# Optimization experiments

Hardware: AMD Instinct MI355X
Metric: run time of the kernel (lower is better)

## Reference

```python
import jax, jax.numpy as jnp
import numpy as np

B, PLEN, D = 32, 1024, 256


def setup_inputs() -> dict:
    key = jax.random.key(0)
    ks = jax.random.split(key, 8)
    u = lambda k, shape: jax.random.uniform(k, shape, jnp.float32, -0.05, 0.05)
    return {
        "P": jax.random.normal(ks[0], (B, PLEN, D), jnp.float32),
        "w_itr_att": u(ks[1], (3 * D,)),
        "w1": u(ks[2], (2 * D, D)),
        "w2": u(ks[3], (2 * D, D)),
        "w3": u(ks[4], (2 * D, D)),
        "b1": u(ks[5], (D,)),
        "b2": u(ks[6], (D,)),
        "b3": u(ks[7], (D,)),
    }


def reference(P, w_itr_att, w1, w2, w3, b1, b2, b3):
    d = P.shape[-1]
    # alpha(a,b) = w_itr_att . [a ; b ; a*b]; split w into the three d-chunks
    wa, wb, wc = w_itr_att[:d], w_itr_att[d:2 * d], w_itr_att[2 * d:]
    # pairwise score A[b,i,j] = wa.P_i + wb.P_j + wc.(P_i * P_j)
    sa = P @ wa                                   # (b, p)
    sb = P @ wb                                   # (b, p)
    A = sa[:, :, None] + sb[:, None, :] + jnp.einsum('bid,bjd->bij', P * wc, P)
    itr_attn = jnp.einsum('bij,bjd->bid', jax.nn.softmax(A, axis=2), P)
    cat = jnp.concatenate([P, itr_attn], axis=-1)  # (b, p, 2d)
    z = jnp.tanh(cat @ w1 + b1)
    r = jax.nn.sigmoid(cat @ w2 + b2)
    f = jax.nn.sigmoid(cat @ w3 + b3)
    return r * P + f * z
```

## Files before the change

kernel.cpp:

```cpp
#include <hip/hip_runtime.h>
#include <hip/hip_bf16.h>

typedef unsigned short u16;
typedef unsigned int   u32;

using bf16x8 = __attribute__((ext_vector_type(8))) short;
using f32x4  = __attribute__((ext_vector_type(4))) float;

#define NB 32
#define NP 1024
#define ND 256

__device__ __forceinline__ u16 f2bf(float x){
  u32 u = __float_as_uint(x);
  u += 0x7FFFu + ((u >> 16) & 1u);
  return (u16)(u >> 16);
}

__device__ __forceinline__ float bf2f(u16 x){
  return __uint_as_float((u32)x << 16);
}

__device__ __forceinline__ void glds16(const void* g, void* l){
  __builtin_amdgcn_global_load_lds((const __attribute__((address_space(1))) void*)g,
                                   (__attribute__((address_space(3))) void*)l, 16, 0, 0);
}

__global__ void prep_rows(const float* __restrict__ P, const float* __restrict__ wi,
                          u16* __restrict__ Pbf, float* __restrict__ sbv){
  const int row  = blockIdx.x * 4 + (threadIdx.x >> 6);
  const int lane = threadIdx.x & 63;
  const float4 p  = *(const float4*)(P  + (size_t)row * ND + lane * 4);
  const float4 wb = *(const float4*)(wi + ND + lane * 4);
  ushort4 pb;
  pb.x = f2bf(p.x); pb.y = f2bf(p.y); pb.z = f2bf(p.z); pb.w = f2bf(p.w);
  *(ushort4*)(Pbf + (size_t)row * ND + lane * 4) = pb;
  float s = p.x*wb.x + p.y*wb.y + p.z*wb.z + p.w*wb.w;
  #pragma unroll
  for (int m = 1; m < 64; m <<= 1) s += __shfl_xor(s, m, 64);
  if (lane == 0) sbv[row] = s;
}

__global__ void prep_w(const float* __restrict__ w1, const float* __restrict__ w2,
                       const float* __restrict__ w3, u16* __restrict__ Wp){
  const int t = blockIdx.x;
  const float* w = (t < 16) ? w1 : ((t < 32) ? w2 : w3);
  const int tid = threadIdx.x;
  #pragma unroll
  for (int j = 0; j < 4; ++j){
    int item = tid + 256 * j;
    int c = item >> 6, lane = item & 63;
    int ncol = ((t & 15) << 4) + (lane & 15);
    int k0 = 32 * c + 8 * (lane >> 4);
    u16 tmp[8];
    #pragma unroll
    for (int e = 0; e < 8; ++e) tmp[e] = f2bf(w[(size_t)(k0 + e) * 256 + ncol]);
    *(uint4*)(Wp + ((size_t)(t * 16 + c) * 64 + lane) * 8) = *(uint4*)tmp;
  }
}

__global__ void transpose_p(const u16* __restrict__ Pbf, u16* __restrict__ PbfT){
  const int b = blockIdx.z, jt = blockIdx.x, dt = blockIdx.y;
  __shared__ u16 T[64][72];
  const int tid = threadIdx.x;
  #pragma unroll
  for (int it = 0; it < 2; ++it){
    int cc = tid + 256 * it;
    int j = cc >> 3, c8 = cc & 7;
    uint4 v = *(const uint4*)(Pbf + ((size_t)b * NP + jt * 64 + j) * ND + dt * 64 + c8 * 8);
    *(uint4*)&T[j][c8 * 8] = v;
  }
  __syncthreads();
  #pragma unroll
  for (int it = 0; it < 2; ++it){
    int cc = tid + 256 * it;
    int d = cc >> 3, c8 = cc & 7;
    u16 tmp[8];
    #pragma unroll
    for (int k = 0; k < 8; ++k) tmp[k] = T[c8 * 8 + k][d];
    *(uint4*)(PbfT + ((size_t)b * ND + dt * 64 + d) * NP + jt * 64 + c8 * 8) = *(uint4*)tmp;
  }
}

__launch_bounds__(128, 2)
__global__ void attn_kernel(const float* __restrict__ P, const float* __restrict__ wi,
                            const u16* __restrict__ Pbf, const u16* __restrict__ PbfT,
                            const float* __restrict__ sbv, u16* __restrict__ attnb){
  const int p    = blockIdx.x;
  const int bid  = ((p & 7) << 7) | (p >> 3);
  const int b    = bid >> 5;
  const int q0   = (bid & 31) << 5;
  const int tid  = threadIdx.x;
  const int wave = tid >> 6, lane = tid & 63, lo = lane & 15, hi = lane >> 4;

  __shared__ __align__(16) u16 KtA[32 * 256];
  __shared__ __align__(16) u16 VtA[256 * 32];
  __shared__ __align__(16) u16 Sp[2][16][40];
  char* KtB = (char*)KtA;
  char* VtB = (char*)VtA;

  bf16x8 qf[8];
  {
    const int qrow = q0 + wave * 16 + lo;
    const float* prow = P  + ((size_t)b * NP + qrow) * ND;
    const float* wcp  = wi + 512;
    #pragma unroll
    for (int c = 0; c < 8; ++c){
      const int d0 = 32 * c + 8 * hi;
      float4 a  = *(const float4*)(prow + d0);
      float4 a2 = *(const float4*)(prow + d0 + 4);
      float4 wa  = *(const float4*)(wcp + d0);
      float4 wa2 = *(const float4*)(wcp + d0 + 4);
      bf16x8 q;
      q[0]=(short)f2bf(a.x*wa.x);  q[1]=(short)f2bf(a.y*wa.y);
      q[2]=(short)f2bf(a.z*wa.z);  q[3]=(short)f2bf(a.w*wa.w);
      q[4]=(short)f2bf(a2.x*wa2.x); q[5]=(short)f2bf(a2.y*wa2.y);
      q[6]=(short)f2bf(a2.z*wa2.z); q[7]=(short)f2bf(a2.w*wa2.w);
      qf[c] = q;
    }
  }

  f32x4 of[16];
  #pragma unroll
  for (int t = 0; t < 16; ++t) of[t] = (f32x4){0.f,0.f,0.f,0.f};
  float mx[4] = {-1e30f,-1e30f,-1e30f,-1e30f};
  float ls[4] = {0.f,0.f,0.f,0.f};

  const u16* kslab = Pbf  + (size_t)b * NP * ND;
  const u16* vslab = PbfT + (size_t)b * ND * NP;

  auto stageK = [&](int kt){
    const int kbase = kt * 32;
    #pragma unroll
    for (int it = 0; it < 8; ++it){
      int off = it * 2048 + tid * 16;
      int j   = off >> 9;
      int ck  = ((off >> 4) & 31) ^ (j & 7);
      glds16((const char*)(kslab + (size_t)(kbase + j) * ND + ck * 8), KtB + off);
    }
  };
  auto stageV = [&](int kt){
    const int kbase = kt * 32;
    #pragma unroll
    for (int it = 0; it < 8; ++it){
      int off = it * 2048 + tid * 16;
      int d   = off >> 6;
      int kc  = ((off >> 4) & 3) ^ (d & 3);
      glds16((const char*)(vslab + (size_t)d * NP + kbase + kc * 8), VtB + off);
    }
  };

  float sbc[2], sbn[2];
  stageK(0);
  stageV(0);
  #pragma unroll
  for (int nt = 0; nt < 2; ++nt) sbc[nt] = sbv[(size_t)b * NP + nt * 16 + lo];
  __syncthreads();

  for (int kt = 0; kt < 32; ++kt){
    f32x4 s[2];
    __builtin_amdgcn_s_setprio(1);
    #pragma unroll
    for (int nt = 0; nt < 2; ++nt){
      f32x4 acc = (f32x4){0.f,0.f,0.f,0.f};
      #pragma unroll
      for (int c = 0; c < 8; ++c){
        int j  = nt * 16 + lo;
        int ad = j * 512 + (((4 * c + hi) ^ (j & 7)) << 4);
        bf16x8 kf = *(const bf16x8*)(KtB + ad);
        acc = __builtin_amdgcn_mfma_f32_16x16x32_bf16(qf[c], kf, acc, 0, 0, 0);
      }
      s[nt] = acc;
    }
    __builtin_amdgcn_s_setprio(0);
    #pragma unroll
    for (int nt = 0; nt < 2; ++nt){
      float sv = sbc[nt];
      #pragma unroll
      for (int r = 0; r < 4; ++r) s[nt][r] += sv;
    }

    __syncthreads();
    if (kt < 31) stageK(kt + 1);

    float md = -1e30f;
    #pragma unroll
    for (int nt = 0; nt < 2; ++nt)
      #pragma unroll
      for (int r = 0; r < 4; ++r) md = fmaxf(md, s[nt][r] - mx[r]);
    if (!__all(md <= 8.f)){
      float scale[4];
      #pragma unroll
      for (int r = 0; r < 4; ++r){
        float v = fmaxf(s[0][r], s[1][r]);
        v = fmaxf(v, __shfl_xor(v, 1, 64));
        v = fmaxf(v, __shfl_xor(v, 2, 64));
        v = fmaxf(v, __shfl_xor(v, 4, 64));
        v = fmaxf(v, __shfl_xor(v, 8, 64));
        float mnew = fmaxf(mx[r], v);
        scale[r] = __expf(mx[r] - mnew);
        mx[r] = mnew;
        ls[r] *= scale[r];
      }
      #pragma unroll
      for (int t = 0; t < 16; ++t)
        #pragma unroll
        for (int r = 0; r < 4; ++r) of[t][r] *= scale[r];
    }
    #pragma unroll
    for (int nt = 0; nt < 2; ++nt)
      #pragma unroll
      for (int r = 0; r < 4; ++r){
        float pv = __expf(s[nt][r] - mx[r]);
        ls[r] += pv;
        Sp[wave][4 * hi + r][16 * nt + lo] = f2bf(pv);
      }

    {
      bf16x8 pa = *(const bf16x8*)&Sp[wave][lo][8 * hi];
      __builtin_amdgcn_s_setprio(1);
      #pragma unroll
      for (int t = 0; t < 16; ++t){
        int d  = 16 * t + lo;
        int ad = d * 64 + ((hi ^ (d & 3)) << 4);
        bf16x8 vb = *(const bf16x8*)(VtB + ad);
        of[t] = __builtin_amdgcn_mfma_f32_16x16x32_bf16(pa, vb, of[t], 0, 0, 0);
      }
      __builtin_amdgcn_s_setprio(0);
    }

    __syncthreads();
    if (kt < 31){
      stageV(kt + 1);
      #pragma unroll
      for (int nt = 0; nt < 2; ++nt)
        sbn[nt] = sbv[(size_t)b * NP + (kt + 1) * 32 + nt * 16 + lo];
      sbc[0] = sbn[0]; sbc[1] = sbn[1];
    }
  }

  #pragma unroll
  for (int r = 0; r < 4; ++r){
    ls[r] += __shfl_xor(ls[r], 1, 64);
    ls[r] += __shfl_xor(ls[r], 2, 64);
    ls[r] += __shfl_xor(ls[r], 4, 64);
    ls[r] += __shfl_xor(ls[r], 8, 64);
  }
  const int qrow = q0 + wave * 16;
  #pragma unroll
  for (int t = 0; t < 16; ++t){
    #pragma unroll
    for (int r = 0; r < 4; ++r){
      float o = of[t][r] / ls[r];
      attnb[((size_t)b * NP + qrow + 4 * hi + r) * ND + 16 * t + lo] = f2bf(o);
    }
  }
}

__launch_bounds__(256, 2)
__global__ void mlp_kernel(const u16* __restrict__ Pbf, const u16* __restrict__ attnb,
                           const u16* __restrict__ Wp,
                           const float* __restrict__ b1, const float* __restrict__ b2,
                           const float* __restrict__ b3, float* __restrict__ out){
  const int p    = blockIdx.x;
  const int swz  = ((p & 7) << 7) | (p >> 3);
  const int mt   = swz >> 2, cg = swz & 3;
  const int tid  = threadIdx.x;
  const int wave = tid >> 6, lane = tid & 63, lo = lane & 15, hi = lane >> 4;
  const int tq   = 4 * cg + wave;
  const int m0   = mt * 128;

  __shared__ __align__(16) u16 Ab[2][128 * 64];

  f32x4 acc[3][8];
  #pragma unroll
  for (int e = 0; e < 3; ++e)
    #pragma unroll
    for (int m = 0; m < 8; ++m) acc[e][m] = (f32x4){0.f,0.f,0.f,0.f};

  auto stage = [&](int s, int buf){
    const u16* xs = (s < 4) ? (Pbf   + (size_t)m0 * ND + s * 64)
                            : (attnb + (size_t)m0 * ND + (s - 4) * 64);
    char* dst = (char*)Ab[buf];
    #pragma unroll
    for (int it = 0; it < 4; ++it){
      int off = it * 4096 + wave * 1024 + lane * 16;
      int row = off >> 7;
      int cl  = (off & 127) ^ ((row & 7) << 4);
      glds16((const char*)(xs + (size_t)row * ND) + cl, dst + it * 4096 + wave * 1024);
    }
  };

  stage(0, 0);
  __syncthreads();

  for (int s = 0; s < 8; ++s){
    if (s < 7) stage(s + 1, (s + 1) & 1);
    const char* ab = (const char*)Ab[s & 1];
    #pragma unroll
    for (int cc = 0; cc < 2; ++cc){
      const int c = 2 * s + cc;
      bf16x8 wf[3];
      #pragma unroll
      for (int e = 0; e < 3; ++e)
        wf[e] = *(const bf16x8*)(Wp + ((size_t)((tq + 16 * e) * 16 + c) * 64 + lane) * 8);
      #pragma unroll
      for (int m = 0; m < 8; ++m){
        int row = 16 * m + lo;
        bf16x8 af = *(const bf16x8*)(ab + row * 128 + ((64 * cc + 16 * hi) ^ ((row & 7) << 4)));
        #pragma unroll
        for (int e = 0; e < 3; ++e)
          acc[e][m] = __builtin_amdgcn_mfma_f32_16x16x32_bf16(af, wf[e], acc[e][m], 0, 0, 0);
      }
    }
    __syncthreads();
  }

  const int d = 16 * tq + lo;
  const float bb1 = b1[d], bb2 = b2[d], bb3 = b3[d];
  #pragma unroll
  for (int m = 0; m < 8; ++m){
    #pragma unroll
    for (int r = 0; r < 4; ++r){
      const int row = m0 + 16 * m + 4 * hi + r;
      float y1 = acc[0][m][r] + bb1;
      float y2 = acc[1][m][r] + bb2;
      float y3 = acc[2][m][r] + bb3;
      float pv = bf2f(Pbf[(size_t)row * ND + d]);
      float e2 = __expf(2.f * y1);
      float z  = (e2 - 1.f) / (e2 + 1.f);
      float rr = 1.f / (1.f + __expf(-y2));
      float ff = 1.f / (1.f + __expf(-y3));
      out[(size_t)row * ND + d] = rr * pv + ff * z;
    }
  }
}

extern "C" void kernel_launch(void* const* d_in, const int* in_sizes, int n_in,
                              void* d_out, int out_size, void* d_ws, size_t ws_size,
                              hipStream_t stream){
  const float* P  = (const float*)d_in[0];
  const float* wi = (const float*)d_in[1];
  const float* w1 = (const float*)d_in[2];
  const float* w2 = (const float*)d_in[3];
  const float* w3 = (const float*)d_in[4];
  const float* b1 = (const float*)d_in[5];
  const float* b2 = (const float*)d_in[6];
  const float* b3 = (const float*)d_in[7];
  float* out = (float*)d_out;

  char* ws = (char*)d_ws;
  u16*   Pbf   = (u16*)  (ws);
  u16*   PbfT  = (u16*)  (ws + (16u << 20));
  u16*   attnb = (u16*)  (ws + (32u << 20));
  u16*   Wp    = (u16*)  (ws + (48u << 20));
  float* sbv   = (float*)(ws + (49u << 20));

  prep_rows<<<8192, 256, 0, stream>>>(P, wi, Pbf, sbv);
  prep_w<<<48, 256, 0, stream>>>(w1, w2, w3, Wp);
  transpose_p<<<dim3(16, 4, 32), 256, 0, stream>>>(Pbf, PbfT);
  attn_kernel<<<1024, 128, 0, stream>>>(P, wi, Pbf, PbfT, sbv, attnb);
  mlp_kernel<<<1024, 256, 0, stream>>>(Pbf, attnb, Wp, b1, b2, b3, out);
}
```

Before: 133.1 us.

## Switch attention to 32x32x16 MFMA with transposed scores and register-resident P

Reworks the attention kernel so each wave handles 32 query rows using 32x32x16 bf16 MFMAs. Scores are computed transposed (keys x queries), which makes the per-query softmax statistics per lane and cuts cross-lane max/sum reductions. Probabilities are repacked into the PV A-operand with lane shuffles instead of a shared-memory round trip. Blocks now cover 64 queries, halving the grid and the number of times K/V tiles are restaged per batch, at the cost of a larger accumulator footprint (128 fp32 per lane) and fewer blocks for the GPU.

```diff
diff --git a/kernel.cpp b/kernel.cpp
--- a/kernel.cpp
+++ b/kernel.cpp
@@ -6,6 +6,7 @@
 
 using bf16x8 = __attribute__((ext_vector_type(8))) short;
 using f32x4  = __attribute__((ext_vector_type(4))) float;
+using f32x16 = __attribute__((ext_vector_type(16))) float;
 
 #define NB 32
 #define NP 1024
@@ -19,6 +20,10 @@
 
 __device__ __forceinline__ float bf2f(u16 x){
   return __uint_as_float((u32)x << 16);
+}
+
+__device__ __forceinline__ u32 packbf(float a, float b){
+  return (u32)f2bf(a) | ((u32)f2bf(b) << 16);
 }
 
 __device__ __forceinline__ void glds16(const void* g, void* l){
@@ -87,44 +92,46 @@
                             const u16* __restrict__ Pbf, const u16* __restrict__ PbfT,
                             const float* __restrict__ sbv, u16* __restrict__ attnb){
   const int p    = blockIdx.x;
-  const int bid  = ((p & 7) << 7) | (p >> 3);
-  const int b    = bid >> 5;
-  const int q0   = (bid & 31) << 5;
+  const int bid  = ((p & 7) << 6) | (p >> 3);
+  const int b    = bid >> 4;
+  const int q0   = (bid & 15) << 6;
   const int tid  = threadIdx.x;
-  const int wave = tid >> 6, lane = tid & 63, lo = lane & 15, hi = lane >> 4;
+  const int wave = tid >> 6, lane = tid & 63;
+  const int q    = lane & 31, hi2 = lane >> 5;
 
   __shared__ __align__(16) u16 KtA[32 * 256];
   __shared__ __align__(16) u16 VtA[256 * 32];
-  __shared__ __align__(16) u16 Sp[2][16][40];
   char* KtB = (char*)KtA;
   char* VtB = (char*)VtA;
 
-  bf16x8 qf[8];
+  bf16x8 qf[16];
   {
-    const int qrow = q0 + wave * 16 + lo;
+    const int qrow = q0 + 32 * wave + q;
     const float* prow = P  + ((size_t)b * NP + qrow) * ND;
     const float* wcp  = wi + 512;
     #pragma unroll
-    for (int c = 0; c < 8; ++c){
-      const int d0 = 32 * c + 8 * hi;
+    for (int ks = 0; ks < 16; ++ks){
+      const int d0 = 16 * ks + 8 * hi2;
       float4 a  = *(const float4*)(prow + d0);
       float4 a2 = *(const float4*)(prow + d0 + 4);
       float4 wa  = *(const float4*)(wcp + d0);
       float4 wa2 = *(const float4*)(wcp + d0 + 4);
-      bf16x8 q;
-      q[0]=(short)f2bf(a.x*wa.x);  q[1]=(short)f2bf(a.y*wa.y);
-      q[2]=(short)f2bf(a.z*wa.z);  q[3]=(short)f2bf(a.w*wa.w);
-      q[4]=(short)f2bf(a2.x*wa2.x); q[5]=(short)f2bf(a2.y*wa2.y);
-      q[6]=(short)f2bf(a2.z*wa2.z); q[7]=(short)f2bf(a2.w*wa2.w);
-      qf[c] = q;
-    }
-  }
-
-  f32x4 of[16];
-  #pragma unroll
-  for (int t = 0; t < 16; ++t) of[t] = (f32x4){0.f,0.f,0.f,0.f};
-  float mx[4] = {-1e30f,-1e30f,-1e30f,-1e30f};
-  float ls[4] = {0.f,0.f,0.f,0.f};
+      bf16x8 qv;
+      qv[0]=(short)f2bf(a.x*wa.x);  qv[1]=(short)f2bf(a.y*wa.y);
+      qv[2]=(short)f2bf(a.z*wa.z);  qv[3]=(short)f2bf(a.w*wa.w);
+      qv[4]=(short)f2bf(a2.x*wa2.x); qv[5]=(short)f2bf(a2.y*wa2.y);
+      qv[6]=(short)f2bf(a2.z*wa2.z); qv[7]=(short)f2bf(a2.w*wa2.w);
+      qf[ks] = qv;
+    }
+  }
+
+  f32x16 of[8];
+  #pragma unroll
+  for (int dt = 0; dt < 8; ++dt)
+    #pragma unroll
+    for (int r = 0; r < 16; ++r) of[dt][r] = 0.f;
+  float mx = -1e30f;
+  float ls = 0.f;
 
   const u16* kslab = Pbf  + (size_t)b * NP * ND;
   const u16* vslab = PbfT + (size_t)b * ND * NP;
@@ -135,8 +142,9 @@
     for (int it = 0; it < 8; ++it){
       int off = it * 2048 + tid * 16;
       int j   = off >> 9;
-      int ck  = ((off >> 4) & 31) ^ (j & 7);
-      glds16((const char*)(kslab + (size_t)(kbase + j) * ND + ck * 8), KtB + off);
+      int u   = (off >> 4) & 31;
+      int d0  = 8 * (u ^ (j & 7));
+      glds16((const char*)(kslab + (size_t)(kbase + j) * ND + d0), KtB + off);
     }
   };
   auto stageV = [&](int kt){
@@ -145,114 +153,94 @@
     for (int it = 0; it < 8; ++it){
       int off = it * 2048 + tid * 16;
       int d   = off >> 6;
-      int kc  = ((off >> 4) & 3) ^ (d & 3);
-      glds16((const char*)(vslab + (size_t)d * NP + kbase + kc * 8), VtB + off);
+      int u   = (off >> 4) & 3;
+      int j0  = 8 * (u ^ (d & 3));
+      glds16((const char*)(vslab + (size_t)d * NP + kbase + j0), VtB + off);
     }
   };
 
-  float sbc[2], sbn[2];
   stageK(0);
   stageV(0);
-  #pragma unroll
-  for (int nt = 0; nt < 2; ++nt) sbc[nt] = sbv[(size_t)b * NP + nt * 16 + lo];
   __syncthreads();
 
   for (int kt = 0; kt < 32; ++kt){
-    f32x4 s[2];
-    __builtin_amdgcn_s_setprio(1);
-    #pragma unroll
-    for (int nt = 0; nt < 2; ++nt){
-      f32x4 acc = (f32x4){0.f,0.f,0.f,0.f};
-      #pragma unroll
-      for (int c = 0; c < 8; ++c){
-        int j  = nt * 16 + lo;
-        int ad = j * 512 + (((4 * c + hi) ^ (j & 7)) << 4);
-        bf16x8 kf = *(const bf16x8*)(KtB + ad);
-        acc = __builtin_amdgcn_mfma_f32_16x16x32_bf16(qf[c], kf, acc, 0, 0, 0);
-      }
-      s[nt] = acc;
-    }
-    __builtin_amdgcn_s_setprio(0);
-    #pragma unroll
-    for (int nt = 0; nt < 2; ++nt){
-      float sv = sbc[nt];
-      #pragma unroll
-      for (int r = 0; r < 4; ++r) s[nt][r] += sv;
-    }
-
+    const int kbase = kt * 32;
+
+    f32x16 s;
+    #pragma unroll
+    for (int r = 0; r < 16; ++r) s[r] = 0.f;
+    #pragma unroll
+    for (int ks = 0; ks < 16; ++ks){
+      int ad = q * 512 + (((2 * ks + hi2) ^ (q & 7)) << 4);
+      bf16x8 kf = *(const bf16x8*)(KtB + ad);
+      s = __builtin_amdgcn_mfma_f32_32x32x16_bf16(kf, qf[ks], s, 0, 0, 0);
+    }
     __syncthreads();
     if (kt < 31) stageK(kt + 1);
 
-    float md = -1e30f;
-    #pragma unroll
-    for (int nt = 0; nt < 2; ++nt)
+    #pragma unroll
+    for (int g = 0; g < 4; ++g){
+      float4 sq = *(const float4*)(sbv + (size_t)b * NP + kbase + 8 * g + 4 * hi2);
+      s[4*g+0] += sq.x; s[4*g+1] += sq.y; s[4*g+2] += sq.z; s[4*g+3] += sq.w;
+    }
+
+    float vmax = s[0];
+    #pragma unroll
+    for (int r = 1; r < 16; ++r) vmax = fmaxf(vmax, s[r]);
+    if (!__all(vmax - mx <= 8.f)){
+      float v = fmaxf(vmax, __shfl_xor(vmax, 32, 64));
+      float mnew = fmaxf(mx, v);
+      float sc = __expf(mx - mnew);
+      mx = mnew; ls *= sc;
       #pragma unroll
-      for (int r = 0; r < 4; ++r) md = fmaxf(md, s[nt][r] - mx[r]);
-    if (!__all(md <= 8.f)){
-      float scale[4];
+      for (int r = 0; r < 16; ++r){
+        float scr = __shfl(sc, (r & 3) + 8 * (r >> 2) + 4 * hi2, 64);
+        #pragma unroll
+        for (int dt = 0; dt < 8; ++dt) of[dt][r] *= scr;
+      }
+    }
+    float E[16];
+    #pragma unroll
+    for (int r = 0; r < 16; ++r){ E[r] = __expf(s[r] - mx); ls += E[r]; }
+
+    #pragma unroll
+    for (int jt = 0; jt < 2; ++jt){
+      u32 a0 = packbf(E[8*jt+0], E[8*jt+1]);
+      u32 a1 = packbf(E[8*jt+2], E[8*jt+3]);
+      u32 b0 = packbf(E[8*jt+4], E[8*jt+5]);
+      u32 b1 = packbf(E[8*jt+6], E[8*jt+7]);
+      u32 ta0 = __shfl_xor((int)a0, 32, 64);
+      u32 ta1 = __shfl_xor((int)a1, 32, 64);
+      u32 tb0 = __shfl_xor((int)b0, 32, 64);
+      u32 tb1 = __shfl_xor((int)b1, 32, 64);
+      union { bf16x8 v; u32 d[4]; } pa;
+      pa.d[0] = hi2 ? tb0 : a0;
+      pa.d[1] = hi2 ? tb1 : a1;
+      pa.d[2] = hi2 ? b0 : ta0;
+      pa.d[3] = hi2 ? b1 : ta1;
       #pragma unroll
-      for (int r = 0; r < 4; ++r){
-        float v = fmaxf(s[0][r], s[1][r]);
-        v = fmaxf(v, __shfl_xor(v, 1, 64));
-        v = fmaxf(v, __shfl_xor(v, 2, 64));
-        v = fmaxf(v, __shfl_xor(v, 4, 64));
-        v = fmaxf(v, __shfl_xor(v, 8, 64));
-        float mnew = fmaxf(mx[r], v);
-        scale[r] = __expf(mx[r] - mnew);
-        mx[r] = mnew;
-        ls[r] *= scale[r];
+      for (int dt = 0; dt < 8; ++dt){
+        int d  = 32 * dt + q;
+        int ad = d * 64 + (((2 * jt + hi2) ^ (d & 3)) << 4);
+        bf16x8 vb = *(const bf16x8*)(VtB + ad);
+        of[dt] = __builtin_amdgcn_mfma_f32_32x32x16_bf16(pa.v, vb, of[dt], 0, 0, 0);
       }
-      #pragma unroll
-      for (int t = 0; t < 16; ++t)
-        #pragma unroll
-        for (int r = 0; r < 4; ++r) of[t][r] *= scale[r];
-    }
-    #pragma unroll
-    for (int nt = 0; nt < 2; ++nt)
-      #pragma unroll
-      for (int r = 0; r < 4; ++r){
-        float pv = __expf(s[nt][r] - mx[r]);
-        ls[r] += pv;
-        Sp[wave][4 * hi + r][16 * nt + lo] = f2bf(pv);
-      }
-
-    {
-      bf16x8 pa = *(const bf16x8*)&Sp[wave][lo][8 * hi];
-      __builtin_amdgcn_s_setprio(1);
-      #pragma unroll
-      for (int t = 0; t < 16; ++t){
-        int d  = 16 * t + lo;
-        int ad = d * 64 + ((hi ^ (d & 3)) << 4);
-        bf16x8 vb = *(const bf16x8*)(VtB + ad);
-        of[t] = __builtin_amdgcn_mfma_f32_16x16x32_bf16(pa, vb, of[t], 0, 0, 0);
-      }
-      __builtin_amdgcn_s_setprio(0);
     }
 
     __syncthreads();
-    if (kt < 31){
-      stageV(kt + 1);
-      #pragma unroll
-      for (int nt = 0; nt < 2; ++nt)
-        sbn[nt] = sbv[(size_t)b * NP + (kt + 1) * 32 + nt * 16 + lo];
-      sbc[0] = sbn[0]; sbc[1] = sbn[1];
-    }
-  }
-
-  #pragma unroll
-  for (int r = 0; r < 4; ++r){
-    ls[r] += __shfl_xor(ls[r], 1, 64);
-    ls[r] += __shfl_xor(ls[r], 2, 64);
-    ls[r] += __shfl_xor(ls[r], 4, 64);
-    ls[r] += __shfl_xor(ls[r], 8, 64);
-  }
-  const int qrow = q0 + wave * 16;
-  #pragma unroll
-  for (int t = 0; t < 16; ++t){
-    #pragma unroll
-    for (int r = 0; r < 4; ++r){
-      float o = of[t][r] / ls[r];
-      attnb[((size_t)b * NP + qrow + 4 * hi + r) * ND + 16 * t + lo] = f2bf(o);
+    if (kt < 31) stageV(kt + 1);
+  }
+
+  ls += __shfl_xor(ls, 32, 64);
+  const int qb = q0 + 32 * wave;
+  #pragma unroll
+  for (int r = 0; r < 16; ++r){
+    const int qr = (r & 3) + 8 * (r >> 2) + 4 * hi2;
+    float lr = __shfl(ls, qr, 64);
+    #pragma unroll
+    for (int dt = 0; dt < 8; ++dt){
+      float o = of[dt][r] / lr;
+      attnb[((size_t)b * NP + qb + qr) * ND + 32 * dt + q] = f2bf(o);
     }
   }
 }
@@ -359,6 +347,6 @@
   prep_rows<<<8192, 256, 0, stream>>>(P, wi, Pbf, sbv);
   prep_w<<<48, 256, 0, stream>>>(w1, w2, w3, Wp);
   transpose_p<<<dim3(16, 4, 32), 256, 0, stream>>>(Pbf, PbfT);
-  attn_kernel<<<1024, 128, 0, stream>>>(P, wi, Pbf, PbfT, sbv, attnb);
+  attn_kernel<<<512, 128, 0, stream>>>(P, wi, Pbf, PbfT, sbv, attnb);
   mlp_kernel<<<1024, 256, 0, stream>>>(Pbf, attnb, Wp, b1, b2, b3, out);
 }
```

New measurement: 246.8 us. 85.5% more time.
